# Optimization experiments

Hardware: AMD Instinct MI355X
Metric: run time of the kernel (lower is better)

Reference implementation:

```python
import jax, jax.numpy as jnp
import numpy as np

BIN_LEN = 0.015625  # quantization bin width from init


def setup_inputs() -> dict:
    key = jax.random.key(0)
    k1, k2, k3 = jax.random.split(key, 3)
    B, NUM_ID, NUM_LVL, D = 64, 256, 64, 10000
    x = jax.random.normal(k1, (B, D), dtype=jnp.float32)
    id_hvs = jax.random.normal(k2, (NUM_ID, D), dtype=jnp.float32)
    lvl_hvs = jax.random.normal(k3, (NUM_LVL, D), dtype=jnp.float32)
    return {"x": x, "id_hvs": id_hvs, "lvl_hvs": lvl_hvs}


def reference(x, id_hvs, lvl_hvs):
    # Fused form of: (x broadcast * id_hvs) @ lvl_hvs^T -> argmax over levels.
    # scores[b, i, l] = sum_d x[b, d] * id_hvs[i, d] * lvl_hvs[l, d]
    scores = jnp.einsum('bd,id,ld->bil', x, id_hvs, lvl_hvs)  # (B, num_id, num_lvl)
    decoded = jnp.argmax(scores, axis=2).astype(jnp.float32) * BIN_LEN  # (B, num_id)
    return decoded
```

## Files before the change

### kernel.cpp

```cpp
#include <hip/hip_runtime.h>


typedef _Float16 f16x8 __attribute__((ext_vector_type(8)));
typedef float f32x4 __attribute__((ext_vector_type(4)));

constexpr int D    = 10000;
constexpr int KPAD = 10016;
constexpr int B    = 64;
constexpr int NI   = 256;
constexpr int NL   = 64;
constexpr int BK   = 32;
constexpr int NCH  = KPAD / BK;
constexpr int S    = 8;
constexpr int BM   = 128;
constexpr float BIN_LEN = 0.015625f;

constexpr size_t OFF_IDH = (size_t)S * B * NI * NL * 4;
constexpr size_t IDSZ    = (size_t)NI * KPAD;

__device__ __forceinline__ float4 ld4(const float* p) {
    return *reinterpret_cast<const float4*>(p);
}

__global__ __launch_bounds__(256)
void hd_split_id(const float* __restrict__ id_hvs,
                 _Float16* __restrict__ idh, _Float16* __restrict__ idl) {
    const int i = blockIdx.x;
    for (int k = threadIdx.x; k < KPAD; k += 256) {
        float v = (k < D) ? id_hvs[(size_t)i * D + k] : 0.0f;
        _Float16 h = (_Float16)v;
        _Float16 lo = (_Float16)(v - (float)h);
        idh[(size_t)i * KPAD + k] = h;
        idl[(size_t)i * KPAD + k] = lo;
    }
}

__global__ __launch_bounds__(256)
void hd_mfma(const float* __restrict__ x, const float* __restrict__ lvl_hvs,
             const _Float16* __restrict__ idh, const _Float16* __restrict__ idl,
             float* __restrict__ part) {
    __shared__ f16x8 sA[2][2][BM][4];
    __shared__ f16x8 sW[2][2][2][NL][4];

    const int tid = threadIdx.x;
    const int bx  = blockIdx.x;
    const int s     = bx >> 6;
    const int ibase = (bx & 1) * BM;
    const int b0    = ((bx >> 1) & 31) * 2;

    const int cb = NCH / S, cr = NCH % S;
    const int cstart = s * cb + (s < cr ? s : cr);
    const int nch    = cb + (s < cr ? 1 : 0);

    const int w_row = (tid >> 2) & 63, w_kg = tid & 3;
    const int w_slot = w_kg ^ ((w_row >> 1) & 3);

    const int wid = tid >> 6;
    const int wm = wid >> 1, wn = wid & 1;
    const int lr = tid & 15, lq = (tid >> 4) & 3;

    f32x4 accM[4][4], accC[4][4];
#pragma unroll
    for (int f = 0; f < 4; ++f)
#pragma unroll
        for (int g = 0; g < 4; ++g) {
            accM[f][g] = (f32x4)0.0f;
            accC[f][g] = (f32x4)0.0f;
        }

    f16x8 r_id[4];
    float r_lv[8], r_x0[8], r_x1[8];

    auto LOAD = [&](int c) {
        const int k0 = (cstart + c) * BK;
#pragma unroll
        for (int m = 0; m < 4; ++m) {
            int u = tid + 256 * m;
            int arr = u >> 9, u2 = u & 511;
            int row = u2 >> 2, kg = u2 & 3;
            const _Float16* src = (arr ? idl : idh)
                + (size_t)(ibase + row) * KPAD + k0 + kg * 8;
            r_id[m] = *reinterpret_cast<const f16x8*>(src);
        }
        {
            const int kb = k0 + w_kg * 8;
            const float* lp  = lvl_hvs + (size_t)w_row * D + kb;
            const float* xp0 = x + (size_t)b0 * D + kb;
            const float* xp1 = xp0 + D;
            if (kb + 8 <= D) {
                float4 a0 = ld4(lp),  a1 = ld4(lp + 4);
                float4 c0 = ld4(xp0), c1 = ld4(xp0 + 4);
                float4 d0 = ld4(xp1), d1 = ld4(xp1 + 4);
                r_lv[0] = a0.x; r_lv[1] = a0.y; r_lv[2] = a0.z; r_lv[3] = a0.w;
                r_lv[4] = a1.x; r_lv[5] = a1.y; r_lv[6] = a1.z; r_lv[7] = a1.w;
                r_x0[0] = c0.x; r_x0[1] = c0.y; r_x0[2] = c0.z; r_x0[3] = c0.w;
                r_x0[4] = c1.x; r_x0[5] = c1.y; r_x0[6] = c1.z; r_x0[7] = c1.w;
                r_x1[0] = d0.x; r_x1[1] = d0.y; r_x1[2] = d0.z; r_x1[3] = d0.w;
                r_x1[4] = d1.x; r_x1[5] = d1.y; r_x1[6] = d1.z; r_x1[7] = d1.w;
            } else {
#pragma unroll
                for (int e = 0; e < 8; ++e) {
                    bool in = (kb + e) < D;
                    r_lv[e] = in ? lp[e]  : 0.0f;
                    r_x0[e] = in ? xp0[e] : 0.0f;
                    r_x1[e] = in ? xp1[e] : 0.0f;
                }
            }
        }
    };

    auto WRITE = [&](int buf) {
#pragma unroll
        for (int m = 0; m < 4; ++m) {
            int u = tid + 256 * m;
            int arr = u >> 9, u2 = u & 511;
            int row = u2 >> 2, kg = u2 & 3;
            sA[buf][arr][row][kg ^ ((row >> 1) & 3)] = r_id[m];
        }
#pragma unroll
        for (int bs = 0; bs < 2; ++bs) {
            const float* rx = bs ? r_x1 : r_x0;
            f16x8 h, lo;
#pragma unroll
            for (int e = 0; e < 8; ++e) {
                float w = rx[e] * r_lv[e];
                _Float16 hh = (_Float16)w;
                h[e] = hh;
                lo[e] = (_Float16)(w - (float)hh);
            }
            sW[buf][0][bs][w_row][w_slot] = h;
            sW[buf][1][bs][w_row][w_slot] = lo;
        }
    };

    auto COMPUTE = [&](int buf) {
        f16x8 bh[4], bl[4];
#pragma unroll
        for (int g = 0; g < 4; ++g) {
            int col = g * 16 + lr;
            int slot = lq ^ ((col >> 1) & 3);
            bh[g] = sW[buf][0][wn][col][slot];
            bl[g] = sW[buf][1][wn][col][slot];
        }
#pragma unroll
        for (int f = 0; f < 4; ++f) {
            int row = wm * 64 + f * 16 + lr;
            int slot = lq ^ ((row >> 1) & 3);
            f16x8 ah = sA[buf][0][row][slot];
            f16x8 al = sA[buf][1][row][slot];
#pragma unroll
            for (int g = 0; g < 4; ++g) {
                accM[f][g] = __builtin_amdgcn_mfma_f32_16x16x32_f16(ah, bh[g], accM[f][g], 0, 0, 0);
                accC[f][g] = __builtin_amdgcn_mfma_f32_16x16x32_f16(ah, bl[g], accC[f][g], 0, 0, 0);
                accC[f][g] = __builtin_amdgcn_mfma_f32_16x16x32_f16(al, bh[g], accC[f][g], 0, 0, 0);
            }
        }
    };

    LOAD(0);
    WRITE(0);
    __syncthreads();

    int cur = 0;
    for (int c = 0; c < nch; ++c) {
        const bool more = (c + 1 < nch);
        if (more) LOAD(c + 1);
        COMPUTE(cur);
        if (more) WRITE(cur ^ 1);
        __syncthreads();
        cur ^= 1;
    }

    float* outp = part + (size_t)(s * B + b0 + wn) * NI * NL;
#pragma unroll
    for (int f = 0; f < 4; ++f) {
#pragma unroll
        for (int g = 0; g < 4; ++g) {
            const int i0 = ibase + wm * 64 + f * 16 + lq * 4;
            const int l  = g * 16 + lr;
#pragma unroll
            for (int r = 0; r < 4; ++r) {
                outp[(size_t)(i0 + r) * NL + l] = accM[f][g][r] + accC[f][g][r];
            }
        }
    }
}

__global__ __launch_bounds__(256)
void hd_phase2(const float* __restrict__ ws, float* __restrict__ out, int SS) {
    const int wid  = blockIdx.x * 4 + (threadIdx.x >> 6);
    const int lane = threadIdx.x & 63;
    const int b = wid >> 8, i = wid & 255;
    const float* p = ws + ((size_t)b * NI + i) * NL + lane;
    const size_t sstride = (size_t)B * NI * NL;

    double s0 = 0.0, s1 = 0.0, s2 = 0.0, s3 = 0.0;
    int ss = 0;
    for (; ss + 4 <= SS; ss += 4) {
        s0 += (double)p[(size_t)(ss + 0) * sstride];
        s1 += (double)p[(size_t)(ss + 1) * sstride];
        s2 += (double)p[(size_t)(ss + 2) * sstride];
        s3 += (double)p[(size_t)(ss + 3) * sstride];
    }
    for (; ss < SS; ++ss) s0 += (double)p[(size_t)ss * sstride];

    double mv = (s0 + s1) + (s2 + s3);
    int mi = lane;
#pragma unroll
    for (int off = 1; off < 64; off <<= 1) {
        double ov = __shfl_xor(mv, off);
        int   oi  = __shfl_xor(mi, off);
        if (ov > mv || (ov == mv && oi < mi)) { mv = ov; mi = oi; }
    }
    if (lane == 0) out[wid] = (float)mi * BIN_LEN;
}

extern "C" void kernel_launch(void* const* d_in, const int* in_sizes, int n_in,
                              void* d_out, int out_size, void* d_ws, size_t ws_size,
                              hipStream_t stream) {
    const float* x       = (const float*)d_in[0];
    const float* id_hvs  = (const float*)d_in[1];
    const float* lvl_hvs = (const float*)d_in[2];
    float* out = (float*)d_out;

    float*     part = (float*)d_ws;
    _Float16*  idh  = (_Float16*)((char*)d_ws + OFF_IDH);
    _Float16*  idl  = idh + IDSZ;

    hd_split_id<<<dim3(NI), dim3(256), 0, stream>>>(id_hvs, idh, idl);
    hd_mfma<<<dim3(S * 64), dim3(256), 0, stream>>>(x, lvl_hvs, idh, idl, part);
    hd_phase2<<<dim3(B * NI / 4), dim3(256), 0, stream>>>(part, out, S);
}
```

Measured before the change: 90.46 us.

## Build lvl*x B-fragments directly in registers instead of via shared memory

Each wave now loads x and lvl_hvs straight from global memory into the register layout the MFMA B-operand needs, then forms the fp16 hi/lo split in registers. This drops the sW shared buffer, its stores and loads, and part of the LDS traffic per chunk. In exchange each thread issues four times as many lvl_hvs loads, since the two waves sharing a wn column, and the two b0 rows, no longer share one staged copy. It also uses more registers, which could lower occupancy.

```diff
diff --git a/kernel.cpp b/kernel.cpp
--- a/kernel.cpp
+++ b/kernel.cpp
@@ -40,7 +40,6 @@
              const _Float16* __restrict__ idh, const _Float16* __restrict__ idl,
              float* __restrict__ part) {
     __shared__ f16x8 sA[2][2][BM][4];
-    __shared__ f16x8 sW[2][2][2][NL][4];
 
     const int tid = threadIdx.x;
     const int bx  = blockIdx.x;
@@ -52,12 +51,10 @@
     const int cstart = s * cb + (s < cr ? s : cr);
     const int nch    = cb + (s < cr ? 1 : 0);
 
-    const int w_row = (tid >> 2) & 63, w_kg = tid & 3;
-    const int w_slot = w_kg ^ ((w_row >> 1) & 3);
-
     const int wid = tid >> 6;
     const int wm = wid >> 1, wn = wid & 1;
     const int lr = tid & 15, lq = (tid >> 4) & 3;
+    const int bq = b0 + wn;
 
     f32x4 accM[4][4], accC[4][4];
 #pragma unroll
@@ -69,9 +66,10 @@
         }
 
     f16x8 r_id[4];
-    float r_lv[8], r_x0[8], r_x1[8];
-
-    auto LOAD = [&](int c) {
+    float rl[4][8], rx[8];
+    f16x8 bh[4], bl[4];
+
+    auto LOAD_A = [&](int c) {
         const int k0 = (cstart + c) * BK;
 #pragma unroll
         for (int m = 0; m < 4; ++m) {
@@ -82,34 +80,9 @@
                 + (size_t)(ibase + row) * KPAD + k0 + kg * 8;
             r_id[m] = *reinterpret_cast<const f16x8*>(src);
         }
-        {
-            const int kb = k0 + w_kg * 8;
-            const float* lp  = lvl_hvs + (size_t)w_row * D + kb;
-            const float* xp0 = x + (size_t)b0 * D + kb;
-            const float* xp1 = xp0 + D;
-            if (kb + 8 <= D) {
-                float4 a0 = ld4(lp),  a1 = ld4(lp + 4);
-                float4 c0 = ld4(xp0), c1 = ld4(xp0 + 4);
-                float4 d0 = ld4(xp1), d1 = ld4(xp1 + 4);
-                r_lv[0] = a0.x; r_lv[1] = a0.y; r_lv[2] = a0.z; r_lv[3] = a0.w;
-                r_lv[4] = a1.x; r_lv[5] = a1.y; r_lv[6] = a1.z; r_lv[7] = a1.w;
-                r_x0[0] = c0.x; r_x0[1] = c0.y; r_x0[2] = c0.z; r_x0[3] = c0.w;
-                r_x0[4] = c1.x; r_x0[5] = c1.y; r_x0[6] = c1.z; r_x0[7] = c1.w;
-                r_x1[0] = d0.x; r_x1[1] = d0.y; r_x1[2] = d0.z; r_x1[3] = d0.w;
-                r_x1[4] = d1.x; r_x1[5] = d1.y; r_x1[6] = d1.z; r_x1[7] = d1.w;
-            } else {
-#pragma unroll
-                for (int e = 0; e < 8; ++e) {
-                    bool in = (kb + e) < D;
-                    r_lv[e] = in ? lp[e]  : 0.0f;
-                    r_x0[e] = in ? xp0[e] : 0.0f;
-                    r_x1[e] = in ? xp1[e] : 0.0f;
-                }
-            }
-        }
-    };
-
-    auto WRITE = [&](int buf) {
+    };
+
+    auto WRITE_A = [&](int buf) {
 #pragma unroll
         for (int m = 0; m < 4; ++m) {
             int u = tid + 256 * m;
@@ -117,31 +90,48 @@
             int row = u2 >> 2, kg = u2 & 3;
             sA[buf][arr][row][kg ^ ((row >> 1) & 3)] = r_id[m];
         }
-#pragma unroll
-        for (int bs = 0; bs < 2; ++bs) {
-            const float* rx = bs ? r_x1 : r_x0;
-            f16x8 h, lo;
+    };
+
+    auto LOAD_W = [&](int c) {
+        const int kb = (cstart + c) * BK + lq * 8;
+        const float* xp = x + (size_t)bq * D + kb;
+        if (kb + 8 <= D) {
+            float4 x0 = ld4(xp), x1 = ld4(xp + 4);
+            rx[0] = x0.x; rx[1] = x0.y; rx[2] = x0.z; rx[3] = x0.w;
+            rx[4] = x1.x; rx[5] = x1.y; rx[6] = x1.z; rx[7] = x1.w;
+#pragma unroll
+            for (int g = 0; g < 4; ++g) {
+                const float* lp = lvl_hvs + (size_t)(g * 16 + lr) * D + kb;
+                float4 a0 = ld4(lp), a1 = ld4(lp + 4);
+                rl[g][0] = a0.x; rl[g][1] = a0.y; rl[g][2] = a0.z; rl[g][3] = a0.w;
+                rl[g][4] = a1.x; rl[g][5] = a1.y; rl[g][6] = a1.z; rl[g][7] = a1.w;
+            }
+        } else {
 #pragma unroll
             for (int e = 0; e < 8; ++e) {
-                float w = rx[e] * r_lv[e];
+                bool in = (kb + e) < D;
+                rx[e] = in ? xp[e] : 0.0f;
+#pragma unroll
+                for (int g = 0; g < 4; ++g)
+                    rl[g][e] = in ? lvl_hvs[(size_t)(g * 16 + lr) * D + kb + e] : 0.0f;
+            }
+        }
+    };
+
+    auto SPLIT = [&]() {
+#pragma unroll
+        for (int g = 0; g < 4; ++g) {
+#pragma unroll
+            for (int e = 0; e < 8; ++e) {
+                float w = rx[e] * rl[g][e];
                 _Float16 hh = (_Float16)w;
-                h[e] = hh;
-                lo[e] = (_Float16)(w - (float)hh);
-            }
-            sW[buf][0][bs][w_row][w_slot] = h;
-            sW[buf][1][bs][w_row][w_slot] = lo;
+                bh[g][e] = hh;
+                bl[g][e] = (_Float16)(w - (float)hh);
+            }
         }
     };
 
     auto COMPUTE = [&](int buf) {
-        f16x8 bh[4], bl[4];
-#pragma unroll
-        for (int g = 0; g < 4; ++g) {
-            int col = g * 16 + lr;
-            int slot = lq ^ ((col >> 1) & 3);
-            bh[g] = sW[buf][0][wn][col][slot];
-            bl[g] = sW[buf][1][wn][col][slot];
-        }
 #pragma unroll
         for (int f = 0; f < 4; ++f) {
             int row = wm * 64 + f * 16 + lr;
@@ -157,21 +147,24 @@
         }
     };
 
-    LOAD(0);
-    WRITE(0);
+    LOAD_W(0);
+    LOAD_A(0);
+    WRITE_A(0);
     __syncthreads();
 
     int cur = 0;
     for (int c = 0; c < nch; ++c) {
         const bool more = (c + 1 < nch);
-        if (more) LOAD(c + 1);
+        if (more) LOAD_A(c + 1);
+        SPLIT();
+        if (more) LOAD_W(c + 1);
         COMPUTE(cur);
-        if (more) WRITE(cur ^ 1);
+        if (more) WRITE_A(cur ^ 1);
         __syncthreads();
         cur ^= 1;
     }
 
-    float* outp = part + (size_t)(s * B + b0 + wn) * NI * NL;
+    float* outp = part + (size_t)(s * B + bq) * NI * NL;
 #pragma unroll
     for (int f = 0; f < 4; ++f) {
 #pragma unroll
```

After: 189.8 us. 2.1x slower.

## Prefetch id tiles two chunks ahead and use lgkm-only barrier

Applied to the files above, without the earlier changes.

Splits the global load stage so the fp16 id-hypervector tiles are prefetched two K-chunks ahead into alternating register sets, while x*lvl products stay one chunk ahead. The loop is unrolled by two to keep register buffers static. __syncthreads is replaced by an explicit lgkmcnt(0) wait plus s_barrier, so the barrier does not also wait on outstanding global loads. This aims to hide global memory latency behind MFMA work, at the cost of more VGPRs that may reduce occupancy.

```diff
diff --git a/kernel.cpp b/kernel.cpp
--- a/kernel.cpp
+++ b/kernel.cpp
@@ -22,6 +22,9 @@
     return *reinterpret_cast<const float4*>(p);
 }
 
+#define LGKM_BAR() do { asm volatile("s_waitcnt lgkmcnt(0)" ::: "memory"); \
+                        __builtin_amdgcn_s_barrier(); } while (0)
+
 __global__ __launch_bounds__(256)
 void hd_split_id(const float* __restrict__ id_hvs,
                  _Float16* __restrict__ idh, _Float16* __restrict__ idl) {
@@ -68,10 +71,10 @@
             accC[f][g] = (f32x4)0.0f;
         }
 
-    f16x8 r_id[4];
+    f16x8 ridE[4], ridO[4];
     float r_lv[8], r_x0[8], r_x1[8];
 
-    auto LOAD = [&](int c) {
+    auto LOAD_A = [&](int c, f16x8 (&rid)[4]) {
         const int k0 = (cstart + c) * BK;
 #pragma unroll
         for (int m = 0; m < 4; ++m) {
@@ -80,43 +83,48 @@
             int row = u2 >> 2, kg = u2 & 3;
             const _Float16* src = (arr ? idl : idh)
                 + (size_t)(ibase + row) * KPAD + k0 + kg * 8;
-            r_id[m] = *reinterpret_cast<const f16x8*>(src);
-        }
-        {
-            const int kb = k0 + w_kg * 8;
-            const float* lp  = lvl_hvs + (size_t)w_row * D + kb;
-            const float* xp0 = x + (size_t)b0 * D + kb;
-            const float* xp1 = xp0 + D;
-            if (kb + 8 <= D) {
-                float4 a0 = ld4(lp),  a1 = ld4(lp + 4);
-                float4 c0 = ld4(xp0), c1 = ld4(xp0 + 4);
-                float4 d0 = ld4(xp1), d1 = ld4(xp1 + 4);
-                r_lv[0] = a0.x; r_lv[1] = a0.y; r_lv[2] = a0.z; r_lv[3] = a0.w;
-                r_lv[4] = a1.x; r_lv[5] = a1.y; r_lv[6] = a1.z; r_lv[7] = a1.w;
-                r_x0[0] = c0.x; r_x0[1] = c0.y; r_x0[2] = c0.z; r_x0[3] = c0.w;
-                r_x0[4] = c1.x; r_x0[5] = c1.y; r_x0[6] = c1.z; r_x0[7] = c1.w;
-                r_x1[0] = d0.x; r_x1[1] = d0.y; r_x1[2] = d0.z; r_x1[3] = d0.w;
-                r_x1[4] = d1.x; r_x1[5] = d1.y; r_x1[6] = d1.z; r_x1[7] = d1.w;
-            } else {
-#pragma unroll
-                for (int e = 0; e < 8; ++e) {
-                    bool in = (kb + e) < D;
-                    r_lv[e] = in ? lp[e]  : 0.0f;
-                    r_x0[e] = in ? xp0[e] : 0.0f;
-                    r_x1[e] = in ? xp1[e] : 0.0f;
-                }
-            }
-        }
-    };
-
-    auto WRITE = [&](int buf) {
+            rid[m] = *reinterpret_cast<const f16x8*>(src);
+        }
+    };
+
+    auto WRITE_A = [&](int buf, f16x8 (&rid)[4]) {
 #pragma unroll
         for (int m = 0; m < 4; ++m) {
             int u = tid + 256 * m;
             int arr = u >> 9, u2 = u & 511;
             int row = u2 >> 2, kg = u2 & 3;
-            sA[buf][arr][row][kg ^ ((row >> 1) & 3)] = r_id[m];
-        }
+            sA[buf][arr][row][kg ^ ((row >> 1) & 3)] = rid[m];
+        }
+    };
+
+    auto LOAD_W = [&](int c) {
+        const int k0 = (cstart + c) * BK;
+        const int kb = k0 + w_kg * 8;
+        const float* lp  = lvl_hvs + (size_t)w_row * D + kb;
+        const float* xp0 = x + (size_t)b0 * D + kb;
+        const float* xp1 = xp0 + D;
+        if (kb + 8 <= D) {
+            float4 a0 = ld4(lp),  a1 = ld4(lp + 4);
+            float4 c0 = ld4(xp0), c1 = ld4(xp0 + 4);
+            float4 d0 = ld4(xp1), d1 = ld4(xp1 + 4);
+            r_lv[0] = a0.x; r_lv[1] = a0.y; r_lv[2] = a0.z; r_lv[3] = a0.w;
+            r_lv[4] = a1.x; r_lv[5] = a1.y; r_lv[6] = a1.z; r_lv[7] = a1.w;
+            r_x0[0] = c0.x; r_x0[1] = c0.y; r_x0[2] = c0.z; r_x0[3] = c0.w;
+            r_x0[4] = c1.x; r_x0[5] = c1.y; r_x0[6] = c1.z; r_x0[7] = c1.w;
+            r_x1[0] = d0.x; r_x1[1] = d0.y; r_x1[2] = d0.z; r_x1[3] = d0.w;
+            r_x1[4] = d1.x; r_x1[5] = d1.y; r_x1[6] = d1.z; r_x1[7] = d1.w;
+        } else {
+#pragma unroll
+            for (int e = 0; e < 8; ++e) {
+                bool in = (kb + e) < D;
+                r_lv[e] = in ? lp[e]  : 0.0f;
+                r_x0[e] = in ? xp0[e] : 0.0f;
+                r_x1[e] = in ? xp1[e] : 0.0f;
+            }
+        }
+    };
+
+    auto WRITE_W = [&](int buf) {
 #pragma unroll
         for (int bs = 0; bs < 2; ++bs) {
             const float* rx = bs ? r_x1 : r_x0;
@@ -157,18 +165,30 @@
         }
     };
 
-    LOAD(0);
-    WRITE(0);
-    __syncthreads();
-
-    int cur = 0;
-    for (int c = 0; c < nch; ++c) {
-        const bool more = (c + 1 < nch);
-        if (more) LOAD(c + 1);
-        COMPUTE(cur);
-        if (more) WRITE(cur ^ 1);
-        __syncthreads();
-        cur ^= 1;
+    LOAD_A(0, ridE);
+    LOAD_W(0);
+    LOAD_A(1, ridO);
+    WRITE_A(0, ridE);
+    WRITE_W(0);
+    LGKM_BAR();
+
+    for (int c = 0; c < nch; c += 2) {
+        {
+            const bool m1 = (c + 1 < nch), m2 = (c + 2 < nch);
+            if (m2) LOAD_A(c + 2, ridE);
+            if (m1) LOAD_W(c + 1);
+            COMPUTE(0);
+            if (m1) { WRITE_A(1, ridO); WRITE_W(1); }
+            LGKM_BAR();
+        }
+        if (c + 1 < nch) {
+            const bool m1 = (c + 2 < nch), m2 = (c + 3 < nch);
+            if (m2) LOAD_A(c + 3, ridO);
+            if (m1) LOAD_W(c + 2);
+            COMPUTE(1);
+            if (m1) { WRITE_A(0, ridE); WRITE_W(0); }
+            LGKM_BAR();
+        }
     }
 
     float* outp = part + (size_t)(s * B + b0 + wn) * NI * NL;
```

Result: slower. 147.4 us (+62.9%).

## Single-buffer LDS tiles and double the K-split count based on workspace size

Applied to the files above, without the earlier changes.

Shared-memory tiles change from double-buffered to single-buffered, with an extra barrier per chunk between compute and the LDS write, which halves LDS use per block so more blocks can share a CU. The split-K factor becomes a runtime value, up to 16 and reduced until the partial buffer fits the workspace, so more blocks are launched on the 256-CU device. The cost is an extra barrier per iteration, less overlap between LDS writes and compute, and twice as much partial-sum traffic for the reduction kernel to read.

```diff
diff --git a/kernel.cpp b/kernel.cpp
--- a/kernel.cpp
+++ b/kernel.cpp
@@ -11,12 +11,10 @@
 constexpr int NL   = 64;
 constexpr int BK   = 32;
 constexpr int NCH  = KPAD / BK;
-constexpr int S    = 8;
 constexpr int BM   = 128;
 constexpr float BIN_LEN = 0.015625f;
 
-constexpr size_t OFF_IDH = (size_t)S * B * NI * NL * 4;
-constexpr size_t IDSZ    = (size_t)NI * KPAD;
+constexpr size_t IDSZ = (size_t)NI * KPAD;
 
 __device__ __forceinline__ float4 ld4(const float* p) {
     return *reinterpret_cast<const float4*>(p);
@@ -38,9 +36,9 @@
 __global__ __launch_bounds__(256)
 void hd_mfma(const float* __restrict__ x, const float* __restrict__ lvl_hvs,
              const _Float16* __restrict__ idh, const _Float16* __restrict__ idl,
-             float* __restrict__ part) {
-    __shared__ f16x8 sA[2][2][BM][4];
-    __shared__ f16x8 sW[2][2][2][NL][4];
+             float* __restrict__ part, int S) {
+    __shared__ f16x8 sA[2][BM][4];
+    __shared__ f16x8 sW[2][2][NL][4];
 
     const int tid = threadIdx.x;
     const int bx  = blockIdx.x;
@@ -71,7 +69,7 @@
     f16x8 r_id[4];
     float r_lv[8], r_x0[8], r_x1[8];
 
-    auto LOAD = [&](int c) {
+    auto LOAD_A = [&](int c) {
         const int k0 = (cstart + c) * BK;
 #pragma unroll
         for (int m = 0; m < 4; ++m) {
@@ -82,41 +80,46 @@
                 + (size_t)(ibase + row) * KPAD + k0 + kg * 8;
             r_id[m] = *reinterpret_cast<const f16x8*>(src);
         }
-        {
-            const int kb = k0 + w_kg * 8;
-            const float* lp  = lvl_hvs + (size_t)w_row * D + kb;
-            const float* xp0 = x + (size_t)b0 * D + kb;
-            const float* xp1 = xp0 + D;
-            if (kb + 8 <= D) {
-                float4 a0 = ld4(lp),  a1 = ld4(lp + 4);
-                float4 c0 = ld4(xp0), c1 = ld4(xp0 + 4);
-                float4 d0 = ld4(xp1), d1 = ld4(xp1 + 4);
-                r_lv[0] = a0.x; r_lv[1] = a0.y; r_lv[2] = a0.z; r_lv[3] = a0.w;
-                r_lv[4] = a1.x; r_lv[5] = a1.y; r_lv[6] = a1.z; r_lv[7] = a1.w;
-                r_x0[0] = c0.x; r_x0[1] = c0.y; r_x0[2] = c0.z; r_x0[3] = c0.w;
-                r_x0[4] = c1.x; r_x0[5] = c1.y; r_x0[6] = c1.z; r_x0[7] = c1.w;
-                r_x1[0] = d0.x; r_x1[1] = d0.y; r_x1[2] = d0.z; r_x1[3] = d0.w;
-                r_x1[4] = d1.x; r_x1[5] = d1.y; r_x1[6] = d1.z; r_x1[7] = d1.w;
-            } else {
-#pragma unroll
-                for (int e = 0; e < 8; ++e) {
-                    bool in = (kb + e) < D;
-                    r_lv[e] = in ? lp[e]  : 0.0f;
-                    r_x0[e] = in ? xp0[e] : 0.0f;
-                    r_x1[e] = in ? xp1[e] : 0.0f;
-                }
-            }
-        }
-    };
-
-    auto WRITE = [&](int buf) {
+    };
+
+    auto WRITE_A = [&]() {
 #pragma unroll
         for (int m = 0; m < 4; ++m) {
             int u = tid + 256 * m;
             int arr = u >> 9, u2 = u & 511;
             int row = u2 >> 2, kg = u2 & 3;
-            sA[buf][arr][row][kg ^ ((row >> 1) & 3)] = r_id[m];
-        }
+            sA[arr][row][kg ^ ((row >> 1) & 3)] = r_id[m];
+        }
+    };
+
+    auto LOAD_W = [&](int c) {
+        const int k0 = (cstart + c) * BK;
+        const int kb = k0 + w_kg * 8;
+        const float* lp  = lvl_hvs + (size_t)w_row * D + kb;
+        const float* xp0 = x + (size_t)b0 * D + kb;
+        const float* xp1 = xp0 + D;
+        if (kb + 8 <= D) {
+            float4 a0 = ld4(lp),  a1 = ld4(lp + 4);
+            float4 c0 = ld4(xp0), c1 = ld4(xp0 + 4);
+            float4 d0 = ld4(xp1), d1 = ld4(xp1 + 4);
+            r_lv[0] = a0.x; r_lv[1] = a0.y; r_lv[2] = a0.z; r_lv[3] = a0.w;
+            r_lv[4] = a1.x; r_lv[5] = a1.y; r_lv[6] = a1.z; r_lv[7] = a1.w;
+            r_x0[0] = c0.x; r_x0[1] = c0.y; r_x0[2] = c0.z; r_x0[3] = c0.w;
+            r_x0[4] = c1.x; r_x0[5] = c1.y; r_x0[6] = c1.z; r_x0[7] = c1.w;
+            r_x1[0] = d0.x; r_x1[1] = d0.y; r_x1[2] = d0.z; r_x1[3] = d0.w;
+            r_x1[4] = d1.x; r_x1[5] = d1.y; r_x1[6] = d1.z; r_x1[7] = d1.w;
+        } else {
+#pragma unroll
+            for (int e = 0; e < 8; ++e) {
+                bool in = (kb + e) < D;
+                r_lv[e] = in ? lp[e]  : 0.0f;
+                r_x0[e] = in ? xp0[e] : 0.0f;
+                r_x1[e] = in ? xp1[e] : 0.0f;
+            }
+        }
+    };
+
+    auto WRITE_W = [&]() {
 #pragma unroll
         for (int bs = 0; bs < 2; ++bs) {
             const float* rx = bs ? r_x1 : r_x0;
@@ -128,26 +131,26 @@
                 h[e] = hh;
                 lo[e] = (_Float16)(w - (float)hh);
             }
-            sW[buf][0][bs][w_row][w_slot] = h;
-            sW[buf][1][bs][w_row][w_slot] = lo;
-        }
-    };
-
-    auto COMPUTE = [&](int buf) {
+            sW[0][bs][w_row][w_slot] = h;
+            sW[1][bs][w_row][w_slot] = lo;
+        }
+    };
+
+    auto COMPUTE = [&]() {
         f16x8 bh[4], bl[4];
 #pragma unroll
         for (int g = 0; g < 4; ++g) {
             int col = g * 16 + lr;
             int slot = lq ^ ((col >> 1) & 3);
-            bh[g] = sW[buf][0][wn][col][slot];
-            bl[g] = sW[buf][1][wn][col][slot];
+            bh[g] = sW[0][wn][col][slot];
+            bl[g] = sW[1][wn][col][slot];
         }
 #pragma unroll
         for (int f = 0; f < 4; ++f) {
             int row = wm * 64 + f * 16 + lr;
             int slot = lq ^ ((row >> 1) & 3);
-            f16x8 ah = sA[buf][0][row][slot];
-            f16x8 al = sA[buf][1][row][slot];
+            f16x8 ah = sA[0][row][slot];
+            f16x8 al = sA[1][row][slot];
 #pragma unroll
             for (int g = 0; g < 4; ++g) {
                 accM[f][g] = __builtin_amdgcn_mfma_f32_16x16x32_f16(ah, bh[g], accM[f][g], 0, 0, 0);
@@ -157,18 +160,19 @@
         }
     };
 
-    LOAD(0);
-    WRITE(0);
+    LOAD_A(0);
+    LOAD_W(0);
+    WRITE_A();
+    WRITE_W();
     __syncthreads();
 
-    int cur = 0;
     for (int c = 0; c < nch; ++c) {
         const bool more = (c + 1 < nch);
-        if (more) LOAD(c + 1);
-        COMPUTE(cur);
-        if (more) WRITE(cur ^ 1);
+        if (more) { LOAD_A(c + 1); LOAD_W(c + 1); }
+        COMPUTE();
         __syncthreads();
-        cur ^= 1;
+        if (more) { WRITE_A(); WRITE_W(); }
+        __syncthreads();
     }
 
     float* outp = part + (size_t)(s * B + b0 + wn) * NI * NL;
@@ -223,11 +227,14 @@
     const float* lvl_hvs = (const float*)d_in[2];
     float* out = (float*)d_out;
 
+    int S = 16;
+    while (S > 1 && ws_size < ((size_t)S << 22) + 2 * IDSZ * sizeof(_Float16)) S >>= 1;
+
     float*     part = (float*)d_ws;
-    _Float16*  idh  = (_Float16*)((char*)d_ws + OFF_IDH);
+    _Float16*  idh  = (_Float16*)((char*)d_ws + ((size_t)S << 22));
     _Float16*  idl  = idh + IDSZ;
 
     hd_split_id<<<dim3(NI), dim3(256), 0, stream>>>(id_hvs, idh, idl);
-    hd_mfma<<<dim3(S * 64), dim3(256), 0, stream>>>(x, lvl_hvs, idh, idl, part);
+    hd_mfma<<<dim3(S * 64), dim3(256), 0, stream>>>(x, lvl_hvs, idh, idl, part, S);
     hd_phase2<<<dim3(B * NI / 4), dim3(256), 0, stream>>>(part, out, S);
 }
```

After: 155.4 us. 1.72x slower.
